# Performance work log

Hardware: AMD Instinct MI355X
Metric: run time of the kernel (lower is better)

The kernel has to match this reference:

```python
import jax, jax.numpy as jnp
import numpy as np

B, T, HM = 2, 2048, 1024
HEADS = 16
DK = (HM // 2) // HEADS   # expand_k = 0.5 -> key_dim 512, per-head 32
DV = HM // HEADS          # expand_v = 1.0 -> per-head 64
LOW_RANK = 16             # gate low-rank dim (fla default)
GATE_NORM = 16.0          # gate_logit_normalizer (fla default)
EPS = 1e-5


def setup_inputs() -> dict:
    key = jax.random.key(0)
    ks = jax.random.split(key, 12)
    def p(k, shape, s=0.02):
        return jax.random.normal(k, shape, jnp.float32) * s
    return dict(
        x=jax.random.normal(ks[0], (B, T, HM), jnp.float32),
        ln_w=jnp.ones((HM,), jnp.float32), ln_b=jnp.zeros((HM,), jnp.float32),
        Wq=p(ks[1], (HM, HEADS * DK)), Wk=p(ks[2], (HM, HEADS * DK)),
        Wv=p(ks[3], (HM, HEADS * DV)),
        gk_w1=p(ks[4], (HM, LOW_RANK)), gk_w2=p(ks[5], (LOW_RANK, HEADS * DK)),
        gk_b2=jnp.zeros((HEADS * DK,), jnp.float32),
        Wg=p(ks[6], (HM, HEADS * DV)), rms_w=jnp.ones((DV,), jnp.float32),
        Wo=p(ks[7], (HEADS * DV, HM)),
        W1=p(ks[8], (HM, 2 * HM)), b1=jnp.zeros((2 * HM,), jnp.float32),
        W2=p(ks[9], (2 * HM, HM)), b2=jnp.zeros((HM,), jnp.float32),
    )


def _ln(x, w, b):
    m = x.mean(-1, keepdims=True)
    v = ((x - m) ** 2).mean(-1, keepdims=True)
    return (x - m) * jax.lax.rsqrt(v + EPS) * w + b


def _rms(x, w):
    return x * jax.lax.rsqrt((x * x).mean(-1, keepdims=True) + EPS) * w


def _gla(q, k, v, gk):
    # gated linear attention recurrence:
    # S_t = diag(exp(gk_t)) S_{t-1} + k_t v_t^T ;  o_t = q_t S_t
    # q,k,gk: [B,T,H,DK], v: [B,T,H,DV]
    def step(S, inp):
        qt, kt, vt, gt = inp
        S = jnp.exp(gt)[..., None] * S + kt[..., None] * vt[..., None, :]
        return S, jnp.einsum('bhk,bhkv->bhv', qt, S)
    xs = tuple(jnp.moveaxis(a, 1, 0) for a in (q, k, v, gk))
    S0 = jnp.zeros((q.shape[0], q.shape[2], q.shape[3], v.shape[3]), q.dtype)
    _, o = jax.lax.scan(step, S0, xs)
    return jnp.moveaxis(o, 0, 1)


def reference(x, ln_w, ln_b, Wq, Wk, Wv, gk_w1, gk_w2, gk_b2, Wg, rms_w, Wo, W1, b1, W2, b2):
    Bb, Tt, _ = x.shape
    h = _ln(x, ln_w, ln_b)
    q = (h @ Wq).reshape(Bb, Tt, HEADS, DK)
    k = (h @ Wk).reshape(Bb, Tt, HEADS, DK)
    v = (h @ Wv).reshape(Bb, Tt, HEADS, DV)
    gk = (jax.nn.log_sigmoid((h @ gk_w1) @ gk_w2 + gk_b2) / GATE_NORM)
    gk = gk.reshape(Bb, Tt, HEADS, DK)
    o = _gla(q * (DK ** -0.5), k, v, gk)
    # output gate: RMSNorm(o) * swish(g)  (FusedRMSNormSwishGate)
    g = (h @ Wg).reshape(Bb, Tt, HEADS, DV)
    o = _rms(o, rms_w) * (g * jax.nn.sigmoid(g))
    x = x + o.reshape(Bb, Tt, HEADS * DV) @ Wo
    h2 = _ln(x, ln_w, ln_b)  # same shared norm module
    return x + jax.nn.gelu(h2 @ W1 + b1, approximate=False) @ W2 + b2
```

## Files before the change

kernel.cpp:

```cpp
#include <hip/hip_runtime.h>
#include <hip/hip_bf16.h>
#include <math.h>


using bf16 = __hip_bfloat16;
typedef __attribute__((ext_vector_type(8))) short bf16x8;
typedef __attribute__((ext_vector_type(4))) float f32x4;

#define BT 4096
#define HM 1024
#define DK 32
#define DV 64
#define NC 32
#define CHK 64

__device__ __forceinline__ float b2f(bf16 v) { return __bfloat162float(v); }
__device__ __forceinline__ bf16 f2b(float v) { return __float2bfloat16(v); }
__device__ __forceinline__ float clampf(float v, float lim) {
    return fminf(fmaxf(v, -lim), lim);
}
__device__ __forceinline__ float lo16(unsigned int u) {
    union { unsigned int i; float f; } c; c.i = u << 16; return c.f;
}
__device__ __forceinline__ float hi16(unsigned int u) {
    union { unsigned int i; float f; } c; c.i = u & 0xffff0000u; return c.f;
}
__device__ __forceinline__ void acc8(float a, uint4 r, float* o) {
    o[0] += a * lo16(r.x); o[1] += a * hi16(r.x);
    o[2] += a * lo16(r.y); o[3] += a * hi16(r.y);
    o[4] += a * lo16(r.z); o[5] += a * hi16(r.z);
    o[6] += a * lo16(r.w); o[7] += a * hi16(r.w);
}

__global__ __launch_bounds__(256) void detect_dtype(
    const unsigned int* __restrict__ x, int* __restrict__ flag)
{
    int tid = threadIdx.x;
    int cnt = 0;
    for (int i = 0; i < 16; ++i) {
        unsigned int w = x[tid * 16 + i];
        unsigned int e_lo = (w >> 7) & 0xffu;
        unsigned int e_hi = (w >> 23) & 0xffu;
        cnt += (e_lo >= 110 && e_lo <= 135 && e_hi >= 110 && e_hi <= 135) ? 1 : 0;
    }
    __shared__ int red[256];
    red[tid] = cnt;
    __syncthreads();
    for (int s = 128; s > 0; s >>= 1) {
        if (tid < s) red[tid] += red[tid + s];
        __syncthreads();
    }
    if (tid == 0) *flag = (red[0] > 2048) ? 1 : 0;
}

__global__ __launch_bounds__(256) void cvt_to_bf16(
    const void* __restrict__ src, bf16* __restrict__ dst, int n,
    const int* __restrict__ flag)
{
    bool isb = (*flag != 0);
    int i = blockIdx.x * 256 + threadIdx.x;
    int stride = gridDim.x * 256;
    for (; i < n; i += stride) {
        if (isb) ((ushort*)dst)[i] = ((const ushort*)src)[i];
        else     dst[i] = f2b(((const float*)src)[i]);
    }
}

__global__ __launch_bounds__(256) void transpose_bf16(
    const ushort* __restrict__ src, ushort* __restrict__ dst, int R, int C)
{
    __shared__ ushort tile[32][33];
    int c0 = blockIdx.x * 32, r0 = blockIdx.y * 32;
    int x = threadIdx.x, y = threadIdx.y;
    #pragma unroll
    for (int dy = 0; dy < 32; dy += 8)
        tile[y + dy][x] = src[(size_t)(r0 + y + dy) * C + c0 + x];
    __syncthreads();
    #pragma unroll
    for (int dy = 0; dy < 32; dy += 8)
        dst[(size_t)(c0 + y + dy) * R + r0 + x] = tile[x][y + dy];
}

template <typename TI>
__global__ __launch_bounds__(256) void ln_kernel(
    const TI* __restrict__ x, const bf16* __restrict__ w, const bf16* __restrict__ b,
    bf16* __restrict__ out)
{
    size_t base = (size_t)blockIdx.x * HM;
    int tid = threadIdx.x;
    float v[4], s = 0.f, s2 = 0.f;
    #pragma unroll
    for (int u = 0; u < 4; ++u) {
        float f;
        if constexpr (sizeof(TI) == 2) f = b2f(((const bf16*)x)[base + tid + u * 256]);
        else                           f = ((const float*)x)[base + tid + u * 256];
        v[u] = f; s += f; s2 += f * f;
    }
    #pragma unroll
    for (int off = 32; off >= 1; off >>= 1) {
        s  += __shfl_down(s, off);
        s2 += __shfl_down(s2, off);
    }
    __shared__ float ra[4], rb[4];
    int wave = tid >> 6;
    if ((tid & 63) == 0) { ra[wave] = s; rb[wave] = s2; }
    __syncthreads();
    s = ra[0] + ra[1] + ra[2] + ra[3];
    s2 = rb[0] + rb[1] + rb[2] + rb[3];
    float mean = s * (1.f / HM);
    float var = fmaxf(s2 * (1.f / HM) - mean * mean, 0.f);
    float rs = rsqrtf(var + 1e-5f);
    #pragma unroll
    for (int u = 0; u < 4; ++u) {
        int col = tid + u * 256;
        out[base + col] = f2b((v[u] - mean) * rs * b2f(w[col]) + b2f(b[col]));
    }
}

__global__ __launch_bounds__(256) void gk_kernel(
    const bf16* __restrict__ h, const bf16* __restrict__ w1,
    const bf16* __restrict__ w2, const bf16* __restrict__ b2i,
    bf16* __restrict__ gkout)
{
    size_t row = blockIdx.x;
    const bf16* hr = h + row * HM;
    int tid = threadIdx.x;
    int d = tid & 15, seg = tid >> 4;
    float s = 0.f;
    for (int j = 0; j < 64; ++j) {
        int i = seg * 64 + j;
        s += b2f(hr[i]) * b2f(w1[i * 16 + d]);
    }
    __shared__ float red[256];
    __shared__ float g1[16];
    red[tid] = s;
    __syncthreads();
    if (tid < 16) {
        float t = 0.f;
        #pragma unroll
        for (int sg = 0; sg < 16; ++sg) t += red[sg * 16 + tid];
        g1[tid] = t;
    }
    __syncthreads();
    #pragma unroll
    for (int rep = 0; rep < 2; ++rep) {
        int n = tid + rep * 256;
        float z = b2f(b2i[n]);
        #pragma unroll
        for (int r = 0; r < 16; ++r) z += g1[r] * b2f(w2[r * 512 + n]);
        z = clampf(z, 30.f);
        float ls = (z >= 0.f) ? -log1pf(expf(-z)) : (z - log1pf(expf(z)));
        gkout[row * 512 + n] = f2b(ls * 0.0625f);
    }
}

template <int MODE>
__global__ __launch_bounds__(256) void gemm_bt(
    const bf16* __restrict__ A, const bf16* __restrict__ Wt,
    const bf16* __restrict__ bias, const void* __restrict__ resid,
    void* __restrict__ out, int M, int N, int K, const int* __restrict__ oflag)
{
    __shared__ __align__(16) ushort As[64][40];
    __shared__ __align__(16) ushort Bs[64][40];
    int tid = threadIdx.x;
    int bm = blockIdx.x * 64, bn = blockIdx.y * 64;
    int wave = tid >> 6, lane = tid & 63;
    int wm = (wave >> 1) * 32, wn = (wave & 1) * 32;
    int row16 = lane & 15, quad = lane >> 4;
    int lr = tid >> 2, lc = (tid & 3) * 8;
    bool out_bf16 = false;
    if constexpr (MODE == 3) out_bf16 = (*oflag != 0);

    f32x4 acc[2][2] = {};
    const ushort* Au = (const ushort*)A;
    const ushort* Wu = (const ushort*)Wt;

    for (int k0 = 0; k0 < K; k0 += 32) {
        __syncthreads();
        *(int4*)&As[lr][lc] = *(const int4*)(Au + (size_t)(bm + lr) * K + k0 + lc);
        *(int4*)&Bs[lr][lc] = *(const int4*)(Wu + (size_t)(bn + lr) * K + k0 + lc);
        __syncthreads();
        #pragma unroll
        for (int mi = 0; mi < 2; ++mi) {
            bf16x8 a = *(const bf16x8*)&As[wm + mi * 16 + row16][quad * 8];
            #pragma unroll
            for (int ni = 0; ni < 2; ++ni) {
                bf16x8 b = *(const bf16x8*)&Bs[wn + ni * 16 + row16][quad * 8];
                acc[mi][ni] = __builtin_amdgcn_mfma_f32_16x16x32_bf16(a, b, acc[mi][ni], 0, 0, 0);
            }
        }
    }
    #pragma unroll
    for (int mi = 0; mi < 2; ++mi) {
        #pragma unroll
        for (int ni = 0; ni < 2; ++ni) {
            int col = bn + wn + ni * 16 + row16;
            #pragma unroll
            for (int r = 0; r < 4; ++r) {
                int row = bm + wm + mi * 16 + quad * 4 + r;
                size_t idx = (size_t)row * N + col;
                float v = acc[mi][ni][r];
                if constexpr (MODE == 0) {
                    ((bf16*)out)[idx] = f2b(clampf(v, 1e4f));
                } else if constexpr (MODE == 1) {
                    ((float*)out)[idx] = clampf(b2f(((const bf16*)resid)[idx]) + v, 1e5f);
                } else if constexpr (MODE == 2) {
                    float t = clampf(v + b2f(bias[col]), 50.f);
                    ((bf16*)out)[idx] = f2b(0.5f * t * (1.f + erff(t * 0.70710678f)));
                } else {
                    float t = clampf(v + b2f(bias[col]) + ((const float*)resid)[idx], 2e5f);
                    if (out_bf16) ((bf16*)out)[idx] = f2b(t);
                    else          ((float*)out)[idx] = t;
                }
            }
        }
    }
}

__global__ __launch_bounds__(256) void gla_phase1(
    const bf16* __restrict__ gkb, const bf16* __restrict__ qk,
    const bf16* __restrict__ vg,
    float* __restrict__ clbuf, float* __restrict__ Dbuf, float* __restrict__ Pbuf)
{
    int bh = blockIdx.x, c = blockIdx.y;
    int b = bh >> 4, hh = bh & 15;
    int row0 = b * 2048 + c * CHK;
    __shared__ float glog[CHK][DK];
    __shared__ float wk[CHK][DK];
    __shared__ __align__(16) ushort vt[CHK][DV];
    int tid = threadIdx.x;
    int i = tid >> 2, k8 = (tid & 3) * 8;
    #pragma unroll
    for (int u = 0; u < 8; ++u) {
        float g = b2f(gkb[(size_t)(row0 + i) * 512 + hh * 32 + k8 + u]);
        glog[i][k8 + u] = fminf(fmaxf(g, -2.f), 0.f);
    }
    {
        int v16 = (tid & 3) * 16;
        #pragma unroll
        for (int u = 0; u < 16; ++u)
            vt[i][v16 + u] = ((const ushort*)vg)[(size_t)(row0 + i) * 2048 + hh * 64 + v16 + u];
    }
    __syncthreads();
    if (tid < 32) {
        float run = 0.f;
        for (int j = 0; j < CHK; ++j) { run += glog[j][tid]; glog[j][tid] = run; }
    }
    __syncthreads();
    #pragma unroll
    for (int u = 0; u < 8; ++u) {
        float cl = glog[i][k8 + u];
        float cl63 = glog[CHK - 1][k8 + u];
        clbuf[(size_t)(row0 + i) * 512 + hh * 32 + k8 + u] = cl;
        wk[i][k8 + u] = expf(fmaxf(cl63 - cl, -60.f)) *
            b2f(qk[(size_t)(row0 + i) * 1024 + 512 + hh * 32 + k8 + u]);
    }
    if (tid < 32) Dbuf[(size_t)(bh * 32 + c) * 32 + tid] = expf(glog[CHK - 1][tid]);
    __syncthreads();
    int kk = tid >> 3, v8 = (tid & 7) * 8;
    float acc[8] = {};
    for (int j = 0; j < CHK; ++j) {
        float w = wk[j][kk];
        uint4 raw = *(const uint4*)&vt[j][v8];
        acc8(w, raw, acc);
    }
    float* Pp = Pbuf + (size_t)(bh * 32 + c) * 2048 + kk * 64 + v8;
    #pragma unroll
    for (int u = 0; u < 8; ++u) Pp[u] = acc[u];
}

__global__ __launch_bounds__(256) void gla_scan(
    const float* __restrict__ Pbuf, const float* __restrict__ Dbuf,
    float* __restrict__ Sbuf)
{
    int bh = blockIdx.x >> 3, vg8 = blockIdx.x & 7;
    int kk = threadIdx.x >> 3, vv = vg8 * 8 + (threadIdx.x & 7);
    float S = 0.f;
    for (int c = 0; c < NC; ++c) {
        size_t idx = (size_t)(bh * 32 + c) * 2048 + kk * 64 + vv;
        float P = Pbuf[idx];
        float D = Dbuf[(size_t)(bh * 32 + c) * 32 + kk];
        Sbuf[idx] = S;
        S = D * S + P;
    }
}

__global__ __launch_bounds__(256) void gla_phase3(
    const bf16* __restrict__ qk, const bf16* __restrict__ vg,
    const float* __restrict__ clbuf, const float* __restrict__ Sbuf,
    const bf16* __restrict__ rmsw, bf16* __restrict__ obuf)
{
    int bh = blockIdx.x, c = blockIdx.y;
    int b = bh >> 4, hh = bh & 15;
    int row0 = b * 2048 + c * CHK;
    __shared__ float qs[CHK][DK], ks[CHK][DK], S0[DK][DV];
    __shared__ float Amat[CHK][CHK];
    __shared__ __align__(16) ushort vt[CHK][DV];
    int tid = threadIdx.x;
    int i = tid >> 2;
    {
        int k8 = (tid & 3) * 8;
        size_t r = (size_t)(row0 + i);
        #pragma unroll
        for (int u = 0; u < 8; ++u) {
            int col = hh * 32 + k8 + u;
            float cl = fmaxf(clbuf[r * 512 + col], -60.f);
            qs[i][k8 + u] = b2f(qk[r * 1024 + col]) * expf(cl) * 0.17677669529663687f;
            ks[i][k8 + u] = b2f(qk[r * 1024 + 512 + col]) * expf(-cl);
        }
        int v16 = (tid & 3) * 16;
        #pragma unroll
        for (int u = 0; u < 16; ++u)
            vt[i][v16 + u] = ((const ushort*)vg)[r * 2048 + hh * 64 + v16 + u];
    }
    {
        int kk = tid >> 3, v8 = (tid & 7) * 8;
        const float* Sp = Sbuf + (size_t)(bh * 32 + c) * 2048 + kk * 64 + v8;
        #pragma unroll
        for (int u = 0; u < 8; ++u) S0[kk][v8 + u] = Sp[u];
    }
    __syncthreads();
    {
        int j0 = (tid & 3) * 16;
        for (int j = j0; j < j0 + 16; ++j) {
            float d = 0.f;
            if (j <= i) {
                const f32x4* qp = (const f32x4*)qs[i];
                const f32x4* kp = (const f32x4*)ks[j];
                #pragma unroll
                for (int q8 = 0; q8 < 8; ++q8) {
                    f32x4 a = qp[q8], bq = kp[q8];
                    d += a.x * bq.x + a.y * bq.y + a.z * bq.z + a.w * bq.w;
                }
            }
            Amat[i][j] = d;
        }
    }
    __syncthreads();
    float o[16] = {};
    int vv = (tid & 3) * 16;
    for (int j = 0; j < CHK; ++j) {
        float a = Amat[i][j];
        uint4 r0 = *(const uint4*)&vt[j][vv];
        uint4 r1 = *(const uint4*)&vt[j][vv + 8];
        acc8(a, r0, o);
        acc8(a, r1, o + 8);
    }
    #pragma unroll
    for (int kk = 0; kk < DK; ++kk) {
        float qv = qs[i][kk];
        const f32x4* Sp = (const f32x4*)&S0[kk][vv];
        #pragma unroll
        for (int q4 = 0; q4 < 4; ++q4) {
            f32x4 sv = Sp[q4];
            o[q4 * 4 + 0] += qv * sv.x; o[q4 * 4 + 1] += qv * sv.y;
            o[q4 * 4 + 2] += qv * sv.z; o[q4 * 4 + 3] += qv * sv.w;
        }
    }
    float ss = 0.f;
    #pragma unroll
    for (int u = 0; u < 16; ++u) ss += o[u] * o[u];
    ss += __shfl_xor(ss, 1);
    ss += __shfl_xor(ss, 2);
    float sc = rsqrtf(fmaxf(ss, 0.f) * (1.f / DV) + 1e-5f);
    size_t r = (size_t)(row0 + i);
    #pragma unroll
    for (int u = 0; u < 16; ++u) {
        float g = b2f(vg[r * 2048 + 1024 + hh * 64 + vv + u]);
        float sw = g / (1.f + expf(-g));
        obuf[r * 1024 + hh * 64 + vv + u] = f2b(clampf(o[u] * sc * b2f(rmsw[vv + u]) * sw, 3e4f));
    }
}

extern "C" void kernel_launch(void* const* d_in, const int* in_sizes, int n_in,
                              void* d_out, int out_size, void* d_ws, size_t ws_size,
                              hipStream_t stream) {
    (void)in_sizes; (void)n_in; (void)out_size; (void)ws_size;

    char* ws = (char*)d_ws;
    const size_t MB = 1024 * 1024;
    const size_t KB = 1024;
    bf16*  WqkT = (bf16*)(ws + 0);
    bf16*  WkT  = (bf16*)(ws + 1 * MB);
    bf16*  WvgT = (bf16*)(ws + 2 * MB);
    bf16*  WgT  = (bf16*)(ws + 4 * MB);
    bf16*  WoT  = (bf16*)(ws + 6 * MB);
    bf16*  W1T  = (bf16*)(ws + 8 * MB);
    bf16*  W2T  = (bf16*)(ws + 12 * MB);
    bf16*  hbuf = (bf16*)(ws + 16 * MB);
    bf16*  qkb  = (bf16*)(ws + 24 * MB);
    bf16*  vgb  = (bf16*)(ws + 32 * MB);
    bf16*  gkb  = (bf16*)(ws + 48 * MB);
    float* clbf = (float*)(ws + 52 * MB);
    float* Dbuf = (float*)(ws + 60 * MB);
    float* Pbuf = (float*)(ws + 61 * MB);
    float* Sbuf = (float*)(ws + 69 * MB);
    bf16*  obuf = (bf16*)(ws + 61 * MB);
    float* ybuf = (float*)(ws + 32 * MB);
    bf16*  f1   = (bf16*)(ws + 48 * MB);
    bf16* cx   = (bf16*)(ws + 77 * MB);
    bf16* cWq  = (bf16*)(ws + 85 * MB);
    bf16* cWk  = (bf16*)(ws + 86 * MB);
    bf16* cWv  = (bf16*)(ws + 87 * MB);
    bf16* cWg  = (bf16*)(ws + 89 * MB);
    bf16* cWo  = (bf16*)(ws + 91 * MB);
    bf16* cW1  = (bf16*)(ws + 93 * MB);
    bf16* cW2  = (bf16*)(ws + 97 * MB);
    bf16* clnw = (bf16*)(ws + 101 * MB);
    bf16* clnb = (bf16*)(ws + 101 * MB + 64 * KB);
    bf16* cgw1 = (bf16*)(ws + 101 * MB + 128 * KB);
    bf16* cgw2 = (bf16*)(ws + 101 * MB + 192 * KB);
    bf16* cgb2 = (bf16*)(ws + 101 * MB + 256 * KB);
    bf16* crms = (bf16*)(ws + 101 * MB + 320 * KB);
    bf16* cb1  = (bf16*)(ws + 101 * MB + 384 * KB);
    bf16* cb2  = (bf16*)(ws + 101 * MB + 448 * KB);
    int*  flag = (int*)(ws + 101 * MB + 512 * KB);

    hipLaunchKernelGGL(detect_dtype, dim3(1), dim3(256), 0, stream,
                       (const unsigned int*)d_in[0], flag);

    struct CV { const void* src; bf16* dst; int n; };
    const CV cvs[16] = {
        { d_in[0],  cx,   4194304 }, { d_in[1],  clnw, 1024 },
        { d_in[2],  clnb, 1024 },    { d_in[3],  cWq,  524288 },
        { d_in[4],  cWk,  524288 },  { d_in[5],  cWv,  1048576 },
        { d_in[6],  cgw1, 16384 },   { d_in[7],  cgw2, 8192 },
        { d_in[8],  cgb2, 512 },     { d_in[9],  cWg,  1048576 },
        { d_in[10], crms, 64 },      { d_in[11], cWo,  1048576 },
        { d_in[12], cW1,  2097152 }, { d_in[13], cb1,  2048 },
        { d_in[14], cW2,  2097152 }, { d_in[15], cb2,  1024 },
    };
    for (int i = 0; i < 16; ++i) {
        int blocks = (cvs[i].n + 255) / 256;
        if (blocks > 2048) blocks = 2048;
        hipLaunchKernelGGL(cvt_to_bf16, dim3(blocks), dim3(256), 0, stream,
                           cvs[i].src, cvs[i].dst, cvs[i].n, flag);
    }

    dim3 tb(32, 8);
    hipLaunchKernelGGL(transpose_bf16, dim3(16, 32), tb, 0, stream, (const ushort*)cWq, (ushort*)WqkT, 1024, 512);
    hipLaunchKernelGGL(transpose_bf16, dim3(16, 32), tb, 0, stream, (const ushort*)cWk, (ushort*)WkT, 1024, 512);
    hipLaunchKernelGGL(transpose_bf16, dim3(32, 32), tb, 0, stream, (const ushort*)cWv, (ushort*)WvgT, 1024, 1024);
    hipLaunchKernelGGL(transpose_bf16, dim3(32, 32), tb, 0, stream, (const ushort*)cWg, (ushort*)WgT, 1024, 1024);
    hipLaunchKernelGGL(transpose_bf16, dim3(32, 32), tb, 0, stream, (const ushort*)cWo, (ushort*)WoT, 1024, 1024);
    hipLaunchKernelGGL(transpose_bf16, dim3(64, 32), tb, 0, stream, (const ushort*)cW1, (ushort*)W1T, 1024, 2048);
    hipLaunchKernelGGL(transpose_bf16, dim3(32, 64), tb, 0, stream, (const ushort*)cW2, (ushort*)W2T, 2048, 1024);

    hipLaunchKernelGGL((ln_kernel<bf16>), dim3(BT), dim3(256), 0, stream, cx, clnw, clnb, hbuf);

    hipLaunchKernelGGL((gemm_bt<0>), dim3(64, 16), dim3(256), 0, stream,
                       hbuf, WqkT, (const bf16*)nullptr, (const void*)nullptr, (void*)qkb, BT, 1024, 1024, (const int*)nullptr);
    hipLaunchKernelGGL((gemm_bt<0>), dim3(64, 32), dim3(256), 0, stream,
                       hbuf, WvgT, (const bf16*)nullptr, (const void*)nullptr, (void*)vgb, BT, 2048, 1024, (const int*)nullptr);
    hipLaunchKernelGGL(gk_kernel, dim3(BT), dim3(256), 0, stream, hbuf, cgw1, cgw2, cgb2, gkb);

    hipLaunchKernelGGL(gla_phase1, dim3(32, 32), dim3(256), 0, stream, gkb, qkb, vgb, clbf, Dbuf, Pbuf);
    hipLaunchKernelGGL(gla_scan, dim3(256), dim3(256), 0, stream, Pbuf, Dbuf, Sbuf);
    hipLaunchKernelGGL(gla_phase3, dim3(32, 32), dim3(256), 0, stream, qkb, vgb, clbf, Sbuf, crms, obuf);

    hipLaunchKernelGGL((gemm_bt<1>), dim3(64, 16), dim3(256), 0, stream,
                       obuf, WoT, (const bf16*)nullptr, (const void*)cx, (void*)ybuf, BT, 1024, 1024, (const int*)nullptr);
    hipLaunchKernelGGL((ln_kernel<float>), dim3(BT), dim3(256), 0, stream, ybuf, clnw, clnb, hbuf);
    hipLaunchKernelGGL((gemm_bt<2>), dim3(64, 32), dim3(256), 0, stream,
                       hbuf, W1T, cb1, (const void*)nullptr, (void*)f1, BT, 2048, 1024, (const int*)nullptr);
    hipLaunchKernelGGL((gemm_bt<3>), dim3(64, 16), dim3(256), 0, stream,
                       f1, W2T, cb2, (const void*)ybuf, d_out, BT, 1024, 2048, flag);
}
```

Before: 466.7 us.

## Enlarge GEMM tiles with direct global-to-LDS loads and fuse weight conversion passes

The GEMM moves from 64x64 to 128x64 block tiles, so each wave computes a 4x2 set of MFMA tiles, and it stages operands through the global_load_lds builtin when that builtin exists. Weight conversion is folded into the transpose kernels, and the many small parameter conversions are batched into one launch, removing about fifteen kernel launches and one pass over the weights. The GLA phase kernels now use padded shared-memory arrays, vectorized uint4 loads of V, and thread mappings chosen to cut bank conflicts and uncoalesced loads. The risks are fewer blocks per GEMM, which lowers occupancy, and an unpadded LDS layout that depends on the fragment ordering matching the direct-load layout.

```diff
diff --git a/kernel.cpp b/kernel.cpp
--- a/kernel.cpp
+++ b/kernel.cpp
@@ -13,6 +13,20 @@
 #define DV 64
 #define NC 32
 #define CHK 64
+
+#if defined(__has_builtin)
+#if __has_builtin(__builtin_amdgcn_global_load_lds)
+#define HAVE_GLDS 1
+#endif
+#endif
+
+#ifdef HAVE_GLDS
+#define GLDS16(g, l) __builtin_amdgcn_global_load_lds( \
+    (const __attribute__((address_space(1))) unsigned int*)(g), \
+    (__attribute__((address_space(3))) unsigned int*)(l), 16, 0, 0)
+#else
+#define GLDS16(g, l) (*(int4*)(l) = *(const int4*)(g))
+#endif
 
 __device__ __forceinline__ float b2f(bf16 v) { return __bfloat162float(v); }
 __device__ __forceinline__ bf16 f2b(float v) { return __float2bfloat16(v); }
@@ -66,15 +80,37 @@
     }
 }
 
-__global__ __launch_bounds__(256) void transpose_bf16(
-    const ushort* __restrict__ src, ushort* __restrict__ dst, int R, int C)
-{
+struct SmallCvt { const void* s[8]; bf16* d[8]; int n[8]; };
+__global__ __launch_bounds__(256) void cvt_small(SmallCvt sc, const int* __restrict__ flag)
+{
+    bool isb = (*flag != 0);
+    int stride = gridDim.x * 256;
+    #pragma unroll
+    for (int seg = 0; seg < 8; ++seg) {
+        int n = sc.n[seg];
+        for (int i = blockIdx.x * 256 + threadIdx.x; i < n; i += stride) {
+            if (isb) ((ushort*)sc.d[seg])[i] = ((const ushort*)sc.s[seg])[i];
+            else     sc.d[seg][i] = f2b(((const float*)sc.s[seg])[i]);
+        }
+    }
+}
+
+__global__ __launch_bounds__(256) void transpose_any(
+    const void* __restrict__ src, ushort* __restrict__ dst, int R, int C,
+    const int* __restrict__ flag)
+{
+    bool isb = (*flag != 0);
     __shared__ ushort tile[32][33];
     int c0 = blockIdx.x * 32, r0 = blockIdx.y * 32;
     int x = threadIdx.x, y = threadIdx.y;
     #pragma unroll
-    for (int dy = 0; dy < 32; dy += 8)
-        tile[y + dy][x] = src[(size_t)(r0 + y + dy) * C + c0 + x];
+    for (int dy = 0; dy < 32; dy += 8) {
+        size_t idx = (size_t)(r0 + y + dy) * C + c0 + x;
+        ushort v;
+        if (isb) v = ((const ushort*)src)[idx];
+        else { bf16 t = f2b(((const float*)src)[idx]); v = *(ushort*)&t; }
+        tile[y + dy][x] = v;
+    }
     __syncthreads();
     #pragma unroll
     for (int dy = 0; dy < 32; dy += 8)
@@ -160,44 +196,56 @@
     const bf16* __restrict__ bias, const void* __restrict__ resid,
     void* __restrict__ out, int M, int N, int K, const int* __restrict__ oflag)
 {
-    __shared__ __align__(16) ushort As[64][40];
-    __shared__ __align__(16) ushort Bs[64][40];
+    __shared__ __align__(16) ushort As[128 * 32];
+    __shared__ __align__(16) ushort Bs[64 * 32];
     int tid = threadIdx.x;
-    int bm = blockIdx.x * 64, bn = blockIdx.y * 64;
-    int wave = tid >> 6, lane = tid & 63;
-    int wm = (wave >> 1) * 32, wn = (wave & 1) * 32;
-    int row16 = lane & 15, quad = lane >> 4;
-    int lr = tid >> 2, lc = (tid & 3) * 8;
+    int w = tid >> 6, l = tid & 63;
+    int bm = blockIdx.x * 128, bn = blockIdx.y * 64;
+    int row16 = l & 15, quad = l >> 4;
     bool out_bf16 = false;
     if constexpr (MODE == 3) out_bf16 = (*oflag != 0);
 
-    f32x4 acc[2][2] = {};
     const ushort* Au = (const ushort*)A;
     const ushort* Wu = (const ushort*)Wt;
-
+    int sr = w * 16 + row16;
+    int scol = quad * 8;
+    const ushort* gA0 = Au + (size_t)(bm + sr) * K + scol;
+    const ushort* gA1 = Au + (size_t)(bm + sr + 64) * K + scol;
+    const ushort* gB0 = Wu + (size_t)(bn + sr) * K + scol;
+    ushort* lA0 = &As[w * 512 + l * 8];
+    ushort* lA1 = &As[2048 + w * 512 + l * 8];
+    ushort* lB0 = &Bs[w * 512 + l * 8];
+
+    int am = (w >> 1) * 4;
+    int an = (w & 1) * 2;
+    int fo = quad * 128 + row16 * 8;
+
+    f32x4 acc[4][2] = {};
     for (int k0 = 0; k0 < K; k0 += 32) {
+        GLDS16(gA0 + k0, lA0);
+        GLDS16(gA1 + k0, lA1);
+        GLDS16(gB0 + k0, lB0);
         __syncthreads();
-        *(int4*)&As[lr][lc] = *(const int4*)(Au + (size_t)(bm + lr) * K + k0 + lc);
-        *(int4*)&Bs[lr][lc] = *(const int4*)(Wu + (size_t)(bn + lr) * K + k0 + lc);
+        bf16x8 af[4], bff[2];
+        #pragma unroll
+        for (int mi = 0; mi < 4; ++mi) af[mi] = *(const bf16x8*)&As[(am + mi) * 512 + fo];
+        #pragma unroll
+        for (int ni = 0; ni < 2; ++ni) bff[ni] = *(const bf16x8*)&Bs[(an + ni) * 512 + fo];
+        #pragma unroll
+        for (int mi = 0; mi < 4; ++mi)
+            #pragma unroll
+            for (int ni = 0; ni < 2; ++ni)
+                acc[mi][ni] = __builtin_amdgcn_mfma_f32_16x16x32_bf16(af[mi], bff[ni], acc[mi][ni], 0, 0, 0);
         __syncthreads();
-        #pragma unroll
-        for (int mi = 0; mi < 2; ++mi) {
-            bf16x8 a = *(const bf16x8*)&As[wm + mi * 16 + row16][quad * 8];
-            #pragma unroll
-            for (int ni = 0; ni < 2; ++ni) {
-                bf16x8 b = *(const bf16x8*)&Bs[wn + ni * 16 + row16][quad * 8];
-                acc[mi][ni] = __builtin_amdgcn_mfma_f32_16x16x32_bf16(a, b, acc[mi][ni], 0, 0, 0);
-            }
-        }
-    }
-    #pragma unroll
-    for (int mi = 0; mi < 2; ++mi) {
+    }
+    #pragma unroll
+    for (int mi = 0; mi < 4; ++mi) {
         #pragma unroll
         for (int ni = 0; ni < 2; ++ni) {
-            int col = bn + wn + ni * 16 + row16;
+            int col = bn + (w & 1) * 32 + ni * 16 + row16;
             #pragma unroll
             for (int r = 0; r < 4; ++r) {
-                int row = bm + wm + mi * 16 + quad * 4 + r;
+                int row = bm + (w >> 1) * 64 + mi * 16 + quad * 4 + r;
                 size_t idx = (size_t)row * N + col;
                 float v = acc[mi][ni][r];
                 if constexpr (MODE == 0) {
@@ -225,21 +273,25 @@
     int bh = blockIdx.x, c = blockIdx.y;
     int b = bh >> 4, hh = bh & 15;
     int row0 = b * 2048 + c * CHK;
-    __shared__ float glog[CHK][DK];
-    __shared__ float wk[CHK][DK];
+    __shared__ float glog[CHK][DK + 1];
+    __shared__ float wk[CHK][DK + 1];
     __shared__ __align__(16) ushort vt[CHK][DV];
     int tid = threadIdx.x;
-    int i = tid >> 2, k8 = (tid & 3) * 8;
+    int k = tid & 31, i8 = (tid >> 5) * 8;
     #pragma unroll
     for (int u = 0; u < 8; ++u) {
-        float g = b2f(gkb[(size_t)(row0 + i) * 512 + hh * 32 + k8 + u]);
-        glog[i][k8 + u] = fminf(fmaxf(g, -2.f), 0.f);
+        int i = i8 + u;
+        float g = b2f(gkb[(size_t)(row0 + i) * 512 + hh * 32 + k]);
+        glog[i][k] = fminf(fmaxf(g, -2.f), 0.f);
     }
     {
-        int v16 = (tid & 3) * 16;
-        #pragma unroll
-        for (int u = 0; u < 16; ++u)
-            vt[i][v16 + u] = ((const ushort*)vg)[(size_t)(row0 + i) * 2048 + hh * 64 + v16 + u];
+        int cc = tid & 7, ii = tid >> 3;
+        #pragma unroll
+        for (int h = 0; h < 2; ++h) {
+            int i = ii + h * 32;
+            uint4 val = *(const uint4*)((const ushort*)vg + (size_t)(row0 + i) * 2048 + hh * 64 + cc * 8);
+            *(uint4*)&vt[i][cc * 8] = val;
+        }
     }
     __syncthreads();
     if (tid < 32) {
@@ -249,11 +301,12 @@
     __syncthreads();
     #pragma unroll
     for (int u = 0; u < 8; ++u) {
-        float cl = glog[i][k8 + u];
-        float cl63 = glog[CHK - 1][k8 + u];
-        clbuf[(size_t)(row0 + i) * 512 + hh * 32 + k8 + u] = cl;
-        wk[i][k8 + u] = expf(fmaxf(cl63 - cl, -60.f)) *
-            b2f(qk[(size_t)(row0 + i) * 1024 + 512 + hh * 32 + k8 + u]);
+        int i = i8 + u;
+        float cl = glog[i][k];
+        float cl63 = glog[CHK - 1][k];
+        clbuf[(size_t)(row0 + i) * 512 + hh * 32 + k] = cl;
+        wk[i][k] = expf(fmaxf(cl63 - cl, -60.f)) *
+            b2f(qk[(size_t)(row0 + i) * 1024 + 512 + hh * 32 + k]);
     }
     if (tid < 32) Dbuf[(size_t)(bh * 32 + c) * 32 + tid] = expf(glog[CHK - 1][tid]);
     __syncthreads();
@@ -293,52 +346,57 @@
     int bh = blockIdx.x, c = blockIdx.y;
     int b = bh >> 4, hh = bh & 15;
     int row0 = b * 2048 + c * CHK;
-    __shared__ float qs[CHK][DK], ks[CHK][DK], S0[DK][DV];
-    __shared__ float Amat[CHK][CHK];
+    __shared__ float qs[CHK][36], ks[CHK][36];
+    __shared__ float S0[DK][68];
+    __shared__ float Amat[CHK][CHK + 1];
     __shared__ __align__(16) ushort vt[CHK][DV];
     int tid = threadIdx.x;
-    int i = tid >> 2;
     {
-        int k8 = (tid & 3) * 8;
-        size_t r = (size_t)(row0 + i);
+        int k = tid & 31, i8 = (tid >> 5) * 8;
         #pragma unroll
         for (int u = 0; u < 8; ++u) {
-            int col = hh * 32 + k8 + u;
+            int i = i8 + u;
+            size_t r = (size_t)(row0 + i);
+            int col = hh * 32 + k;
             float cl = fmaxf(clbuf[r * 512 + col], -60.f);
-            qs[i][k8 + u] = b2f(qk[r * 1024 + col]) * expf(cl) * 0.17677669529663687f;
-            ks[i][k8 + u] = b2f(qk[r * 1024 + 512 + col]) * expf(-cl);
-        }
-        int v16 = (tid & 3) * 16;
-        #pragma unroll
-        for (int u = 0; u < 16; ++u)
-            vt[i][v16 + u] = ((const ushort*)vg)[r * 2048 + hh * 64 + v16 + u];
+            qs[i][k] = b2f(qk[r * 1024 + col]) * expf(cl) * 0.17677669529663687f;
+            ks[i][k] = b2f(qk[r * 1024 + 512 + col]) * expf(-cl);
+        }
+    }
+    {
+        int cc = tid & 7, ii = tid >> 3;
+        #pragma unroll
+        for (int h = 0; h < 2; ++h) {
+            int i = ii + h * 32;
+            uint4 val = *(const uint4*)((const ushort*)vg + (size_t)(row0 + i) * 2048 + hh * 64 + cc * 8);
+            *(uint4*)&vt[i][cc * 8] = val;
+        }
     }
     {
         int kk = tid >> 3, v8 = (tid & 7) * 8;
         const float* Sp = Sbuf + (size_t)(bh * 32 + c) * 2048 + kk * 64 + v8;
-        #pragma unroll
-        for (int u = 0; u < 8; ++u) S0[kk][v8 + u] = Sp[u];
-    }
-    __syncthreads();
-    {
-        int j0 = (tid & 3) * 16;
-        for (int j = j0; j < j0 + 16; ++j) {
-            float d = 0.f;
-            if (j <= i) {
-                const f32x4* qp = (const f32x4*)qs[i];
-                const f32x4* kp = (const f32x4*)ks[j];
-                #pragma unroll
-                for (int q8 = 0; q8 < 8; ++q8) {
-                    f32x4 a = qp[q8], bq = kp[q8];
-                    d += a.x * bq.x + a.y * bq.y + a.z * bq.z + a.w * bq.w;
-                }
+        *(f32x4*)&S0[kk][v8]     = *(const f32x4*)Sp;
+        *(f32x4*)&S0[kk][v8 + 4] = *(const f32x4*)(Sp + 4);
+    }
+    __syncthreads();
+    int i = tid >> 2, jb = tid & 3;
+    for (int jj = 0; jj < 16; ++jj) {
+        int j = jb + jj * 4;
+        float d = 0.f;
+        if (j <= i) {
+            const f32x4* qp = (const f32x4*)qs[i];
+            const f32x4* kp = (const f32x4*)ks[j];
+            #pragma unroll
+            for (int q8 = 0; q8 < 8; ++q8) {
+                f32x4 a = qp[q8], bq = kp[q8];
+                d += a.x * bq.x + a.y * bq.y + a.z * bq.z + a.w * bq.w;
             }
-            Amat[i][j] = d;
-        }
+        }
+        Amat[i][j] = d;
     }
     __syncthreads();
     float o[16] = {};
-    int vv = (tid & 3) * 16;
+    int vv = jb * 16;
     for (int j = 0; j < CHK; ++j) {
         float a = Amat[i][j];
         uint4 r0 = *(const uint4*)&vt[j][vv];
@@ -398,59 +456,47 @@
     bf16*  obuf = (bf16*)(ws + 61 * MB);
     float* ybuf = (float*)(ws + 32 * MB);
     bf16*  f1   = (bf16*)(ws + 48 * MB);
-    bf16* cx   = (bf16*)(ws + 77 * MB);
-    bf16* cWq  = (bf16*)(ws + 85 * MB);
-    bf16* cWk  = (bf16*)(ws + 86 * MB);
-    bf16* cWv  = (bf16*)(ws + 87 * MB);
-    bf16* cWg  = (bf16*)(ws + 89 * MB);
-    bf16* cWo  = (bf16*)(ws + 91 * MB);
-    bf16* cW1  = (bf16*)(ws + 93 * MB);
-    bf16* cW2  = (bf16*)(ws + 97 * MB);
-    bf16* clnw = (bf16*)(ws + 101 * MB);
-    bf16* clnb = (bf16*)(ws + 101 * MB + 64 * KB);
-    bf16* cgw1 = (bf16*)(ws + 101 * MB + 128 * KB);
-    bf16* cgw2 = (bf16*)(ws + 101 * MB + 192 * KB);
-    bf16* cgb2 = (bf16*)(ws + 101 * MB + 256 * KB);
-    bf16* crms = (bf16*)(ws + 101 * MB + 320 * KB);
-    bf16* cb1  = (bf16*)(ws + 101 * MB + 384 * KB);
-    bf16* cb2  = (bf16*)(ws + 101 * MB + 448 * KB);
-    int*  flag = (int*)(ws + 101 * MB + 512 * KB);
+    bf16*  cx   = (bf16*)(ws + 77 * MB);
+    bf16*  clnw = (bf16*)(ws + 85 * MB);
+    bf16*  clnb = (bf16*)(ws + 85 * MB + 64 * KB);
+    bf16*  cgw1 = (bf16*)(ws + 85 * MB + 128 * KB);
+    bf16*  cgw2 = (bf16*)(ws + 85 * MB + 192 * KB);
+    bf16*  cgb2 = (bf16*)(ws + 85 * MB + 256 * KB);
+    bf16*  crms = (bf16*)(ws + 85 * MB + 320 * KB);
+    bf16*  cb1  = (bf16*)(ws + 85 * MB + 384 * KB);
+    bf16*  cb2  = (bf16*)(ws + 85 * MB + 448 * KB);
+    int*   flag = (int*)(ws + 85 * MB + 512 * KB);
 
     hipLaunchKernelGGL(detect_dtype, dim3(1), dim3(256), 0, stream,
                        (const unsigned int*)d_in[0], flag);
 
-    struct CV { const void* src; bf16* dst; int n; };
-    const CV cvs[16] = {
-        { d_in[0],  cx,   4194304 }, { d_in[1],  clnw, 1024 },
-        { d_in[2],  clnb, 1024 },    { d_in[3],  cWq,  524288 },
-        { d_in[4],  cWk,  524288 },  { d_in[5],  cWv,  1048576 },
-        { d_in[6],  cgw1, 16384 },   { d_in[7],  cgw2, 8192 },
-        { d_in[8],  cgb2, 512 },     { d_in[9],  cWg,  1048576 },
-        { d_in[10], crms, 64 },      { d_in[11], cWo,  1048576 },
-        { d_in[12], cW1,  2097152 }, { d_in[13], cb1,  2048 },
-        { d_in[14], cW2,  2097152 }, { d_in[15], cb2,  1024 },
-    };
-    for (int i = 0; i < 16; ++i) {
-        int blocks = (cvs[i].n + 255) / 256;
-        if (blocks > 2048) blocks = 2048;
-        hipLaunchKernelGGL(cvt_to_bf16, dim3(blocks), dim3(256), 0, stream,
-                           cvs[i].src, cvs[i].dst, cvs[i].n, flag);
-    }
+    hipLaunchKernelGGL(cvt_to_bf16, dim3(2048), dim3(256), 0, stream,
+                       d_in[0], cx, 4194304, flag);
+    SmallCvt sc;
+    sc.s[0] = d_in[1];  sc.d[0] = clnw; sc.n[0] = 1024;
+    sc.s[1] = d_in[2];  sc.d[1] = clnb; sc.n[1] = 1024;
+    sc.s[2] = d_in[6];  sc.d[2] = cgw1; sc.n[2] = 16384;
+    sc.s[3] = d_in[7];  sc.d[3] = cgw2; sc.n[3] = 8192;
+    sc.s[4] = d_in[8];  sc.d[4] = cgb2; sc.n[4] = 512;
+    sc.s[5] = d_in[10]; sc.d[5] = crms; sc.n[5] = 64;
+    sc.s[6] = d_in[13]; sc.d[6] = cb1;  sc.n[6] = 2048;
+    sc.s[7] = d_in[15]; sc.d[7] = cb2;  sc.n[7] = 1024;
+    hipLaunchKernelGGL(cvt_small, dim3(64), dim3(256), 0, stream, sc, flag);
 
     dim3 tb(32, 8);
-    hipLaunchKernelGGL(transpose_bf16, dim3(16, 32), tb, 0, stream, (const ushort*)cWq, (ushort*)WqkT, 1024, 512);
-    hipLaunchKernelGGL(transpose_bf16, dim3(16, 32), tb, 0, stream, (const ushort*)cWk, (ushort*)WkT, 1024, 512);
-    hipLaunchKernelGGL(transpose_bf16, dim3(32, 32), tb, 0, stream, (const ushort*)cWv, (ushort*)WvgT, 1024, 1024);
-    hipLaunchKernelGGL(transpose_bf16, dim3(32, 32), tb, 0, stream, (const ushort*)cWg, (ushort*)WgT, 1024, 1024);
-    hipLaunchKernelGGL(transpose_bf16, dim3(32, 32), tb, 0, stream, (const ushort*)cWo, (ushort*)WoT, 1024, 1024);
-    hipLaunchKernelGGL(transpose_bf16, dim3(64, 32), tb, 0, stream, (const ushort*)cW1, (ushort*)W1T, 1024, 2048);
-    hipLaunchKernelGGL(transpose_bf16, dim3(32, 64), tb, 0, stream, (const ushort*)cW2, (ushort*)W2T, 2048, 1024);
+    hipLaunchKernelGGL(transpose_any, dim3(16, 32), tb, 0, stream, d_in[3],  (ushort*)WqkT, 1024, 512, flag);
+    hipLaunchKernelGGL(transpose_any, dim3(16, 32), tb, 0, stream, d_in[4],  (ushort*)WkT,  1024, 512, flag);
+    hipLaunchKernelGGL(transpose_any, dim3(32, 32), tb, 0, stream, d_in[5],  (ushort*)WvgT, 1024, 1024, flag);
+    hipLaunchKernelGGL(transpose_any, dim3(32, 32), tb, 0, stream, d_in[9],  (ushort*)WgT,  1024, 1024, flag);
+    hipLaunchKernelGGL(transpose_any, dim3(32, 32), tb, 0, stream, d_in[11], (ushort*)WoT,  1024, 1024, flag);
+    hipLaunchKernelGGL(transpose_any, dim3(64, 32), tb, 0, stream, d_in[12], (ushort*)W1T,  1024, 2048, flag);
+    hipLaunchKernelGGL(transpose_any, dim3(32, 64), tb, 0, stream, d_in[14], (ushort*)W2T,  2048, 1024, flag);
 
     hipLaunchKernelGGL((ln_kernel<bf16>), dim3(BT), dim3(256), 0, stream, cx, clnw, clnb, hbuf);
 
-    hipLaunchKernelGGL((gemm_bt<0>), dim3(64, 16), dim3(256), 0, stream,
+    hipLaunchKernelGGL((gemm_bt<0>), dim3(32, 16), dim3(256), 0, stream,
                        hbuf, WqkT, (const bf16*)nullptr, (const void*)nullptr, (void*)qkb, BT, 1024, 1024, (const int*)nullptr);
-    hipLaunchKernelGGL((gemm_bt<0>), dim3(64, 32), dim3(256), 0, stream,
+    hipLaunchKernelGGL((gemm_bt<0>), dim3(32, 32), dim3(256), 0, stream,
                        hbuf, WvgT, (const bf16*)nullptr, (const void*)nullptr, (void*)vgb, BT, 2048, 1024, (const int*)nullptr);
     hipLaunchKernelGGL(gk_kernel, dim3(BT), dim3(256), 0, stream, hbuf, cgw1, cgw2, cgb2, gkb);
 
@@ -458,11 +504,11 @@
     hipLaunchKernelGGL(gla_scan, dim3(256), dim3(256), 0, stream, Pbuf, Dbuf, Sbuf);
     hipLaunchKernelGGL(gla_phase3, dim3(32, 32), dim3(256), 0, stream, qkb, vgb, clbf, Sbuf, crms, obuf);
 
-    hipLaunchKernelGGL((gemm_bt<1>), dim3(64, 16), dim3(256), 0, stream,
+    hipLaunchKernelGGL((gemm_bt<1>), dim3(32, 16), dim3(256), 0, stream,
                        obuf, WoT, (const bf16*)nullptr, (const void*)cx, (void*)ybuf, BT, 1024, 1024, (const int*)nullptr);
     hipLaunchKernelGGL((ln_kernel<float>), dim3(BT), dim3(256), 0, stream, ybuf, clnw, clnb, hbuf);
-    hipLaunchKernelGGL((gemm_bt<2>), dim3(64, 32), dim3(256), 0, stream,
+    hipLaunchKernelGGL((gemm_bt<2>), dim3(32, 32), dim3(256), 0, stream,
                        hbuf, W1T, cb1, (const void*)nullptr, (void*)f1, BT, 2048, 1024, (const int*)nullptr);
-    hipLaunchKernelGGL((gemm_bt<3>), dim3(64, 16), dim3(256), 0, stream,
+    hipLaunchKernelGGL((gemm_bt<3>), dim3(32, 16), dim3(256), 0, stream,
                        f1, W2T, cb2, (const void*)ybuf, d_out, BT, 1024, 2048, flag);
 }
```

Result: no change. 459.5 us (-1.6%).
